# Kernel tuning notes

Hardware: AMD Instinct MI355X
Metric: run time of the kernel (lower is better)

## Reference

```python
import jax, jax.numpy as jnp
import numpy as np

TOP_K = 2
CAPACITY_FACTOR = 1.0


def _ffn(x, w1, w2):
    # SwiGLU FFN: x [N, D], w1 [D, 2F], w2 [F, D]
    h = x @ w1
    x1, x2 = jnp.split(h, 2, axis=-1)
    return (x1 * jax.nn.silu(x2)) @ w2


def setup_inputs() -> dict:
    key = jax.random.key(0)
    ks = jax.random.split(key, 6)
    B, S, D, F, E_r, E_s = 4, 2048, 2048, 1024, 7, 1
    sc_in = 1.0 / np.sqrt(D)
    sc_mid = 1.0 / np.sqrt(F)
    return {
        "x": jax.random.normal(ks[0], (B, S, D), dtype=jnp.float32),
        "gate_w": jax.random.normal(ks[1], (D, E_r), dtype=jnp.float32) * sc_in,
        "expert_bias": jnp.zeros((E_r,), dtype=jnp.float32),
        "shared_w1": jax.random.normal(ks[2], (E_s, D, 2 * F), dtype=jnp.float32) * sc_in,
        "shared_w2": jax.random.normal(ks[3], (E_s, F, D), dtype=jnp.float32) * sc_mid,
        "routed_w1": jax.random.normal(ks[4], (E_r, D, 2 * F), dtype=jnp.float32) * sc_in,
        "routed_w2": jax.random.normal(ks[5], (E_r, F, D), dtype=jnp.float32) * sc_mid,
    }


def reference(x, gate_w, expert_bias, shared_w1, shared_w2, routed_w1, routed_w2):
    B, S, D = x.shape
    E_r = gate_w.shape[1]
    T = B * S
    capacity = max(1, int(CAPACITY_FACTOR * T / E_r))
    flat_x = x.reshape(T, D)

    # shared experts: applied to every token, summed
    shared_sum = jax.vmap(_ffn, in_axes=(None, 0, 0))(flat_x, shared_w1, shared_w2).sum(0)

    # gating (eval mode: no noise, no dropout)
    gate_logits = flat_x @ gate_w + expert_bias  # [T, E_r]
    aff = jax.nn.sigmoid(gate_logits)
    _, topk_idx = jax.lax.top_k(aff, TOP_K)  # [T, K]
    # mask[t, e] = expert e is among token t's top-k
    mask = (topk_idx[:, :, None] == jnp.arange(E_r)[None, None, :]).any(axis=1)  # [T, E_r]

    # per-expert capacity selection: keep top-`capacity` masked tokens by affinity
    score = jnp.where(mask, aff, -1.0).T  # [E_r, T]; aff >= 0 so -1 sorts last
    _, sel_idx = jax.lax.top_k(score, capacity)  # [E_r, capacity] token ids
    kept = jnp.take_along_axis(mask.T, sel_idx, axis=1)  # [E_r, cap]
    w = jnp.where(kept, jnp.take_along_axis(aff.T, sel_idx, axis=1), 0.0)  # [E_r, cap]

    # grouped gather -> FFN -> weighted scatter-add
    inp = flat_x[sel_idx]  # [E_r, cap, D]
    out = jax.vmap(_ffn)(inp, routed_w1, routed_w2)  # [E_r, cap, D]
    routed_sum = jnp.zeros_like(flat_x).at[sel_idx].add(out * w[:, :, None])

    return (shared_sum + routed_sum).reshape(B, S, D)
```

## Files before the change

kernel.cpp:

```cpp
#include <hip/hip_runtime.h>
#include <hip/hip_bf16.h>

typedef unsigned long long u64;
typedef __bf16 bf16x8 __attribute__((ext_vector_type(8)));
typedef float f32x4 __attribute__((ext_vector_type(4)));
typedef unsigned short ushort8_t __attribute__((ext_vector_type(8)));

#define TOKS 8192
#define DMODEL 2048
#define FD 1024
#define NEXP 7
#define CAP 1170
#define CAPP 1280

#define MFMA16(a, b, c) __builtin_amdgcn_mfma_f32_16x16x32_bf16(a, b, c, 0, 0, 0)

__device__ __forceinline__ unsigned short f2bf(float f) {
  __hip_bfloat16 b = __float2bfloat16(f);
  return __builtin_bit_cast(unsigned short, b);
}
__device__ __forceinline__ float bf2f(unsigned short u) {
  __hip_bfloat16 b = __builtin_bit_cast(__hip_bfloat16, u);
  return __bfloat162float(b);
}
__device__ __forceinline__ void gload_lds16(const void* g, void* l) {
  __builtin_amdgcn_global_load_lds(
      (const __attribute__((address_space(1))) void*)g,
      (__attribute__((address_space(3))) void*)l, 16, 0, 0);
}

__global__ void k_convert_x(const float* __restrict__ x,
                            unsigned short* __restrict__ xb, long n4) {
  long i = (long)blockIdx.x * blockDim.x + threadIdx.x;
  long stride = (long)gridDim.x * blockDim.x;
  for (; i < n4; i += stride) {
    float4 v = ((const float4*)x)[i];
    ushort4 o;
    o.x = f2bf(v.x); o.y = f2bf(v.y); o.z = f2bf(v.z); o.w = f2bf(v.w);
    ((ushort4*)xb)[i] = o;
  }
}

template <bool PERM>
__global__ void k_transpose_bf16(const float* __restrict__ in0,
                                 const float* __restrict__ inr,
                                 unsigned short* __restrict__ out,
                                 int R, int C) {
  __shared__ float tile[32][33];
  int z = blockIdx.z;
  const float* in = (z == 0) ? in0 : (inr + (long)(z - 1) * R * C);
  unsigned short* o = out + (long)z * R * C;
  int c0 = blockIdx.x * 32;
  int r0 = blockIdx.y * 32;
  int tx = threadIdx.x, ty = threadIdx.y;
#pragma unroll
  for (int k = 0; k < 4; ++k)
    tile[ty + 8 * k][tx] = in[(long)(r0 + ty + 8 * k) * C + c0 + tx];
  __syncthreads();
#pragma unroll
  for (int k = 0; k < 4; ++k) {
    int c = c0 + ty + 8 * k;
    long orow = PERM ? (long)(((c & 1023) >> 4) * 32 + ((c >> 10) << 4) + (c & 15))
                     : (long)c;
    o[orow * R + r0 + tx] = f2bf(tile[tx][ty + 8 * k]);
  }
}

__global__ void k_gating(const float* __restrict__ x,
                         const float* __restrict__ gw,
                         const float* __restrict__ bias,
                         u64* __restrict__ keys) {
  int wave = threadIdx.x >> 6;
  int lane = threadIdx.x & 63;
  int t = blockIdx.x * 4 + wave;
  const float* xr = x + (long)t * DMODEL;
  double acc[NEXP];
#pragma unroll
  for (int e = 0; e < NEXP; ++e) acc[e] = 0.0;
  for (int i = lane; i < DMODEL; i += 64) {
    double xv = (double)xr[i];
    const float* g = gw + (long)i * NEXP;
#pragma unroll
    for (int e = 0; e < NEXP; ++e) acc[e] += xv * (double)g[e];
  }
#pragma unroll
  for (int e = 0; e < NEXP; ++e) {
    for (int off = 32; off > 0; off >>= 1)
      acc[e] += __shfl_down(acc[e], off, 64);
  }
  if (lane == 0) {
    float aff[NEXP];
#pragma unroll
    for (int e = 0; e < NEXP; ++e) {
      double lg = acc[e] + (double)bias[e];
      aff[e] = (float)(1.0 / (1.0 + exp(-lg)));
    }
    int i1 = 0;
    for (int e = 1; e < NEXP; ++e) if (aff[e] > aff[i1]) i1 = e;
    int i2 = -1;
    for (int e = 0; e < NEXP; ++e) {
      if (e == i1) continue;
      if (i2 < 0 || aff[e] > aff[i2]) i2 = e;
    }
#pragma unroll
    for (int e = 0; e < NEXP; ++e) {
      u64 key = (u64)(0xFFFFFFFFu - (unsigned)t);
      if (e == i1 || e == i2) key |= ((u64)__float_as_uint(aff[e])) << 32;
      keys[(long)e * TOKS + t] = key;
    }
  }
}

__global__ __launch_bounds__(1024) void k_select(
    const u64* __restrict__ keys, int* __restrict__ sel,
    float* __restrict__ selw) {
  __shared__ unsigned hist[256];
  __shared__ u64 s_prefix;
  __shared__ unsigned s_k;
  __shared__ unsigned s_cnt;
  const int e = blockIdx.x;
  const u64* kk = keys + (long)e * TOKS;
  const int tid = threadIdx.x;
  if (tid == 0) { s_prefix = 0; s_k = CAP; s_cnt = 0; }
  __syncthreads();
  for (int shift = 56; shift >= 0; shift -= 8) {
    if (tid < 256) hist[tid] = 0;
    __syncthreads();
    u64 pref = s_prefix;
    for (int i = tid; i < TOKS; i += 1024) {
      u64 key = kk[i];
      bool match = (shift == 56) || ((key >> (shift + 8)) == pref);
      if (match) atomicAdd(&hist[(unsigned)(key >> shift) & 255u], 1u);
    }
    __syncthreads();
    if (tid == 0) {
      unsigned k = s_k, cum = 0;
      for (int b = 255; b >= 0; --b) {
        unsigned c = hist[b];
        if (cum + c >= k) {
          s_prefix = (s_prefix << 8) | (unsigned)b;
          s_k = k - cum;
          break;
        }
        cum += c;
      }
    }
    __syncthreads();
  }
  const u64 T = s_prefix;
  for (int i = tid; i < TOKS; i += 1024) {
    u64 key = kk[i];
    if (key >= T) {
      unsigned p = atomicAdd(&s_cnt, 1u);
      int tok = (int)(0xFFFFFFFFu - (unsigned)(key & 0xFFFFFFFFull));
      unsigned vb = (unsigned)(key >> 32);
      sel[e * CAPP + p] = tok;
      selw[e * CAPP + p] = vb ? __uint_as_float(vb) : 0.0f;
    }
  }
  for (int i = CAP + tid; i < CAPP; i += 1024) {
    sel[e * CAPP + i] = 0;
    selw[e * CAPP + i] = 0.0f;
  }
}

template <int EPI, bool GATHER>
__global__ __launch_bounds__(512, 2) void k_gemm2ph(
    const unsigned short* __restrict__ Abase,
    const unsigned short* __restrict__ Bbase,
    unsigned short* __restrict__ Cbf, float* __restrict__ Cf32,
    const int* __restrict__ sel, const float* __restrict__ selw,
    int N, int K, long strideA, long strideB, long strideC) {
  extern __shared__ unsigned short lds[];
  const int tid = threadIdx.x;
  const int w = tid >> 6;
  const int lane = tid & 63;

  long lin = blockIdx.x + (long)gridDim.x * (blockIdx.y + (long)gridDim.y * blockIdx.z);
  long nwg = (long)gridDim.x * gridDim.y * gridDim.z;
  long swz = (lin & 7) * (nwg >> 3) + (lin >> 3);
  int bx = (int)(swz % gridDim.x);
  long rem = swz / gridDim.x;
  int by = (int)(rem % gridDim.y);
  int z = (int)(rem / gridDim.y);

  const long m0 = (long)by * 256;
  const long n0 = (long)bx * 256;
  const unsigned short* A = Abase + (GATHER ? 0L : (long)z * strideA);
  const unsigned short* Bm = Bbase + (long)z * strideB;

  const int wr = w >> 2;
  const int wc = w & 3;
  const int lr = lane & 15;
  const int kq = lane >> 4;

  const int srow = (w << 3) + (lane >> 3);
  const int scol = (((lane & 7) ^ (lane >> 3)) << 3);
  const unsigned short* aPtr[4];
  const unsigned short* bPtr[4];
#pragma unroll
  for (int j = 0; j < 4; ++j) {
    int r = j * 64 + srow;
    long ar = GATHER ? (long)sel[z * CAPP + (int)m0 + r] : (m0 + r);
    aPtr[j] = A + ar * (long)K + scol;
    bPtr[j] = Bm + (n0 + r) * (long)K + scol;
  }
  const int dst0 = tid * 8;

  auto STAGE = [&](int buf, int t) {
    unsigned short* base = lds + buf * 32768;
    const long ko = (long)t * 64;
#pragma unroll
    for (int j = 0; j < 4; ++j) {
      gload_lds16(aPtr[j] + ko, base + j * 4096 + dst0);
      gload_lds16(bPtr[j] + ko, base + 16384 + j * 4096 + dst0);
    }
  };

  const int slot0 = (kq ^ (lr & 7)) * 8;
  const int slot1 = ((kq + 4) ^ (lr & 7)) * 8;
  const int aRow = wr * 128 + lr;
  const int bRow = wc * 64 + lr;

  const int nk = K >> 6;

  STAGE(0, 0);
  asm volatile("s_waitcnt vmcnt(0)" ::: "memory");
  __builtin_amdgcn_sched_barrier(0);
  __builtin_amdgcn_s_barrier();
  __builtin_amdgcn_sched_barrier(0);

  f32x4 acc[8][4] = {};
  int cur = 0;

#pragma unroll 1
  for (int t = 0; t < nk; ++t) {
    if (t + 1 < nk) STAGE(cur ^ 1, t + 1);
    const unsigned short* aSeg = lds + cur * 32768;
    const unsigned short* bSeg = aSeg + 16384;
    bf16x8 af[8], bf[4];
#pragma unroll
    for (int m = 0; m < 8; ++m)
      af[m] = *(const bf16x8*)&aSeg[(aRow + m * 16) * 64 + slot0];
#pragma unroll
    for (int n = 0; n < 4; ++n)
      bf[n] = *(const bf16x8*)&bSeg[(bRow + n * 16) * 64 + slot0];
    asm volatile("s_waitcnt lgkmcnt(0)" ::: "memory");
    __builtin_amdgcn_sched_barrier(0);
    __builtin_amdgcn_s_setprio(1);
#pragma unroll
    for (int m = 0; m < 8; ++m)
#pragma unroll
      for (int n = 0; n < 4; ++n)
        acc[m][n] = MFMA16(af[m], bf[n], acc[m][n]);
    __builtin_amdgcn_s_setprio(0);
#pragma unroll
    for (int m = 0; m < 8; ++m)
      af[m] = *(const bf16x8*)&aSeg[(aRow + m * 16) * 64 + slot1];
#pragma unroll
    for (int n = 0; n < 4; ++n)
      bf[n] = *(const bf16x8*)&bSeg[(bRow + n * 16) * 64 + slot1];
    asm volatile("s_waitcnt lgkmcnt(0)" ::: "memory");
    __builtin_amdgcn_sched_barrier(0);
    __builtin_amdgcn_s_setprio(1);
#pragma unroll
    for (int m = 0; m < 8; ++m)
#pragma unroll
      for (int n = 0; n < 4; ++n)
        acc[m][n] = MFMA16(af[m], bf[n], acc[m][n]);
    __builtin_amdgcn_s_setprio(0);
    asm volatile("s_waitcnt vmcnt(0)" ::: "memory");
    __builtin_amdgcn_sched_barrier(0);
    __builtin_amdgcn_s_barrier();
    __builtin_amdgcn_sched_barrier(0);
    cur ^= 1;
  }

  const int r0q = (lane >> 4) * 4;
  const int cc = lane & 15;
  const long crow0 = m0 + wr * 128;
  const long ccol0 = n0 + wc * 64;

  if (EPI == 1) {
#pragma unroll
    for (int m = 0; m < 8; ++m)
#pragma unroll
      for (int r = 0; r < 4; ++r) {
        long row = crow0 + m * 16 + r0q + r;
#pragma unroll
        for (int n = 0; n < 4; ++n)
          Cf32[row * N + ccol0 + n * 16 + cc] = acc[m][n][r];
      }
  } else if (EPI == 2) {
#pragma unroll
    for (int m = 0; m < 8; ++m)
#pragma unroll
      for (int r = 0; r < 4; ++r) {
        int srowi = (int)crow0 + m * 16 + r0q + r;
        int tok = sel[z * CAPP + srowi];
        float wgt = selw[z * CAPP + srowi];
        if (wgt != 0.0f) {
#pragma unroll
          for (int n = 0; n < 4; ++n)
            atomicAdd(&Cf32[(long)tok * N + ccol0 + n * 16 + cc],
                      acc[m][n][r] * wgt);
        }
      }
  } else {
    unsigned short* C = Cbf + (long)z * strideC;
    const int halfN = N >> 1;
    const long gcol0 = (ccol0 >> 1);
#pragma unroll
    for (int m = 0; m < 8; ++m)
#pragma unroll
      for (int r = 0; r < 4; ++r) {
        long row = crow0 + m * 16 + r0q + r;
#pragma unroll
        for (int q = 0; q < 2; ++q) {
          float x1v = acc[m][2 * q][r];
          float x2v = acc[m][2 * q + 1][r];
          float s = x2v / (1.0f + __expf(-x2v));
          C[row * halfN + gcol0 + q * 16 + cc] = f2bf(x1v * s);
        }
      }
  }
}

extern "C" void kernel_launch(void* const* d_in, const int* in_sizes, int n_in,
                              void* d_out, int out_size, void* d_ws,
                              size_t ws_size, hipStream_t stream) {
  (void)in_sizes; (void)n_in; (void)out_size; (void)ws_size;
  const float* x = (const float*)d_in[0];
  const float* gw = (const float*)d_in[1];
  const float* eb = (const float*)d_in[2];
  const float* sw1 = (const float*)d_in[3];
  const float* sw2 = (const float*)d_in[4];
  const float* rw1 = (const float*)d_in[5];
  const float* rw2 = (const float*)d_in[6];
  float* out = (float*)d_out;

  char* ws = (char*)d_ws;
  size_t off = 0;
  auto alloc = [&](size_t bytes) {
    size_t o = off;
    off += (bytes + 255) & ~(size_t)255;
    return o;
  };
  unsigned short* xb  = (unsigned short*)(ws + alloc((size_t)TOKS * DMODEL * 2));
  unsigned short* w1t = (unsigned short*)(ws + alloc((size_t)8 * DMODEL * (2 * FD) * 2));
  unsigned short* w2t = (unsigned short*)(ws + alloc((size_t)8 * DMODEL * FD * 2));
  unsigned short* a_sh = (unsigned short*)(ws + alloc((size_t)TOKS * FD * 2));
  unsigned short* a_r  = (unsigned short*)(ws + alloc((size_t)NEXP * CAPP * FD * 2));
  u64* keys = (u64*)(ws + alloc((size_t)NEXP * TOKS * 8));
  int* sel  = (int*)(ws + alloc((size_t)NEXP * CAPP * 4));
  float* selw = (float*)(ws + alloc((size_t)NEXP * CAPP * 4));

  const size_t LDSB = 131072;

  k_convert_x<<<8192, 256, 0, stream>>>(x, xb, (long)TOKS * DMODEL / 4);
  dim3 tb(32, 8);
  k_transpose_bf16<true><<<dim3(64, 64, 8), tb, 0, stream>>>(sw1, rw1, w1t, DMODEL, 2 * FD);
  k_transpose_bf16<false><<<dim3(64, 32, 8), tb, 0, stream>>>(sw2, rw2, w2t, FD, DMODEL);
  k_gating<<<TOKS / 4, 256, 0, stream>>>(x, gw, eb, keys);
  k_select<<<NEXP, 1024, 0, stream>>>(keys, sel, selw);
  k_gemm2ph<3, false><<<dim3(8, 32, 1), 512, LDSB, stream>>>(
      xb, w1t, a_sh, nullptr, nullptr, nullptr, 2 * FD, DMODEL, 0, 0, 0);
  k_gemm2ph<1, false><<<dim3(8, 32, 1), 512, LDSB, stream>>>(
      a_sh, w2t, nullptr, out, nullptr, nullptr, DMODEL, FD, 0, 0, 0);
  k_gemm2ph<3, true><<<dim3(8, CAPP / 256, NEXP), 512, LDSB, stream>>>(
      xb, w1t + (size_t)DMODEL * (2 * FD), a_r, nullptr, sel, nullptr, 2 * FD,
      DMODEL, 0, (long)DMODEL * (2 * FD), (long)CAPP * FD);
  k_gemm2ph<2, false><<<dim3(8, CAPP / 256, NEXP), 512, LDSB, stream>>>(
      a_r, w2t + (size_t)DMODEL * FD, nullptr, out, sel, selw, DMODEL, FD,
      (long)CAPP * FD, (long)DMODEL * FD, 0);
}
```

Measured before the change: 531.2 us.

## Shrink GEMM tiles to 128x128 and replace atomic scatter with deterministic combine

The GEMM kernel moves from 256x256 tiles with 512 threads and 128KB of dynamic LDS to 128x128 tiles with 256 threads, a K-step of 32 and static LDS, so more blocks fit per CU and the grids get more blocks. The routed down-projection no longer atomically adds weighted rows into the output. It writes weighted bf16 rows to a buffer. k_select now builds a per-token inverse map, and a new combine kernel adds the one or two routed rows into the output. This trades scattered fp32 atomics for an extra write and read pass plus a memset, and it rounds the routed outputs to bf16 before they are summed.

```diff
diff --git a/kernel.cpp b/kernel.cpp
--- a/kernel.cpp
+++ b/kernel.cpp
@@ -113,7 +113,8 @@
 
 __global__ __launch_bounds__(1024) void k_select(
     const u64* __restrict__ keys, int* __restrict__ sel,
-    float* __restrict__ selw) {
+    float* __restrict__ selw, unsigned* __restrict__ cnt,
+    int* __restrict__ inv) {
   __shared__ unsigned hist[256];
   __shared__ u64 s_prefix;
   __shared__ unsigned s_k;
@@ -156,6 +157,10 @@
       unsigned vb = (unsigned)(key >> 32);
       sel[e * CAPP + p] = tok;
       selw[e * CAPP + p] = vb ? __uint_as_float(vb) : 0.0f;
+      if (vb) {
+        unsigned pos = atomicAdd(&cnt[tok], 1u);
+        inv[tok * 2 + pos] = e * CAPP + (int)p;
+      }
     }
   }
   for (int i = CAP + tid; i < CAPP; i += 1024) {
@@ -164,14 +169,41 @@
   }
 }
 
+__global__ __launch_bounds__(256) void k_combine(
+    float* __restrict__ out, const unsigned short* __restrict__ rout,
+    const int* __restrict__ inv, const unsigned* __restrict__ cnt) {
+  const int tok = blockIdx.x;
+  const unsigned c = cnt[tok];
+  if (c == 0) return;
+  int i0 = inv[tok * 2];
+  int i1 = (c > 1) ? inv[tok * 2 + 1] : -1;
+  if (c > 1 && i1 < i0) { int t = i0; i0 = i1; i1 = t; }
+  const int col = threadIdx.x * 8;
+  float* o = out + (long)tok * DMODEL + col;
+  float4 v0 = *(float4*)o;
+  float4 v1 = *(float4*)(o + 4);
+  ushort8_t r0 = *(const ushort8_t*)&rout[(long)i0 * DMODEL + col];
+#pragma unroll
+  for (int j = 0; j < 4; ++j) { v0.x; }
+  v0.x += bf2f(r0[0]); v0.y += bf2f(r0[1]); v0.z += bf2f(r0[2]); v0.w += bf2f(r0[3]);
+  v1.x += bf2f(r0[4]); v1.y += bf2f(r0[5]); v1.z += bf2f(r0[6]); v1.w += bf2f(r0[7]);
+  if (c > 1) {
+    ushort8_t r1 = *(const ushort8_t*)&rout[(long)i1 * DMODEL + col];
+    v0.x += bf2f(r1[0]); v0.y += bf2f(r1[1]); v0.z += bf2f(r1[2]); v0.w += bf2f(r1[3]);
+    v1.x += bf2f(r1[4]); v1.y += bf2f(r1[5]); v1.z += bf2f(r1[6]); v1.w += bf2f(r1[7]);
+  }
+  *(float4*)o = v0;
+  *(float4*)(o + 4) = v1;
+}
+
 template <int EPI, bool GATHER>
-__global__ __launch_bounds__(512, 2) void k_gemm2ph(
+__global__ __launch_bounds__(256, 4) void k_gemm128(
     const unsigned short* __restrict__ Abase,
     const unsigned short* __restrict__ Bbase,
     unsigned short* __restrict__ Cbf, float* __restrict__ Cf32,
     const int* __restrict__ sel, const float* __restrict__ selw,
     int N, int K, long strideA, long strideB, long strideC) {
-  extern __shared__ unsigned short lds[];
+  __shared__ unsigned short lds[2][8192];
   const int tid = threadIdx.x;
   const int w = tid >> 6;
   const int lane = tid & 63;
@@ -184,45 +216,45 @@
   int by = (int)(rem % gridDim.y);
   int z = (int)(rem / gridDim.y);
 
-  const long m0 = (long)by * 256;
-  const long n0 = (long)bx * 256;
+  const long m0 = (long)by * 128;
+  const long n0 = (long)bx * 128;
   const unsigned short* A = Abase + (GATHER ? 0L : (long)z * strideA);
   const unsigned short* Bm = Bbase + (long)z * strideB;
 
-  const int wr = w >> 2;
-  const int wc = w & 3;
+  const int wr = w >> 1;
+  const int wc = w & 1;
   const int lr = lane & 15;
   const int kq = lane >> 4;
 
-  const int srow = (w << 3) + (lane >> 3);
-  const int scol = (((lane & 7) ^ (lane >> 3)) << 3);
-  const unsigned short* aPtr[4];
-  const unsigned short* bPtr[4];
-#pragma unroll
-  for (int j = 0; j < 4; ++j) {
-    int r = j * 64 + srow;
+  const int r_ = (w << 4) + (lane >> 2);
+  const int p_ = lane & 3;
+  const unsigned short* aSrc[2];
+  const unsigned short* bSrc[2];
+#pragma unroll
+  for (int c = 0; c < 2; ++c) {
+    int r = c * 64 + r_;
+    int q = p_ ^ ((r & 3) ^ ((r >> 2) & 3));
     long ar = GATHER ? (long)sel[z * CAPP + (int)m0 + r] : (m0 + r);
-    aPtr[j] = A + ar * (long)K + scol;
-    bPtr[j] = Bm + (n0 + r) * (long)K + scol;
+    aSrc[c] = A + ar * (long)K + q * 8;
+    bSrc[c] = Bm + (n0 + r) * (long)K + q * 8;
   }
   const int dst0 = tid * 8;
 
   auto STAGE = [&](int buf, int t) {
-    unsigned short* base = lds + buf * 32768;
-    const long ko = (long)t * 64;
-#pragma unroll
-    for (int j = 0; j < 4; ++j) {
-      gload_lds16(aPtr[j] + ko, base + j * 4096 + dst0);
-      gload_lds16(bPtr[j] + ko, base + 16384 + j * 4096 + dst0);
+    const long ko = (long)t * 32;
+#pragma unroll
+    for (int c = 0; c < 2; ++c) {
+      gload_lds16(aSrc[c] + ko, &lds[buf][c * 2048 + dst0]);
+      gload_lds16(bSrc[c] + ko, &lds[buf][4096 + c * 2048 + dst0]);
     }
   };
 
-  const int slot0 = (kq ^ (lr & 7)) * 8;
-  const int slot1 = ((kq + 4) ^ (lr & 7)) * 8;
-  const int aRow = wr * 128 + lr;
+  const int gl = (lr & 3) ^ ((lr >> 2) & 3);
+  const int slot = (kq ^ gl) * 8;
+  const int aRow = wr * 64 + lr;
   const int bRow = wc * 64 + lr;
 
-  const int nk = K >> 6;
+  const int nk = K >> 5;
 
   STAGE(0, 0);
   asm volatile("s_waitcnt vmcnt(0)" ::: "memory");
@@ -230,41 +262,26 @@
   __builtin_amdgcn_s_barrier();
   __builtin_amdgcn_sched_barrier(0);
 
-  f32x4 acc[8][4] = {};
+  f32x4 acc[4][4] = {};
   int cur = 0;
 
 #pragma unroll 1
   for (int t = 0; t < nk; ++t) {
     if (t + 1 < nk) STAGE(cur ^ 1, t + 1);
-    const unsigned short* aSeg = lds + cur * 32768;
-    const unsigned short* bSeg = aSeg + 16384;
-    bf16x8 af[8], bf[4];
-#pragma unroll
-    for (int m = 0; m < 8; ++m)
-      af[m] = *(const bf16x8*)&aSeg[(aRow + m * 16) * 64 + slot0];
+    const unsigned short* aSeg = &lds[cur][0];
+    const unsigned short* bSeg = &lds[cur][4096];
+    bf16x8 af[4], bf[4];
+#pragma unroll
+    for (int m = 0; m < 4; ++m)
+      af[m] = *(const bf16x8*)&aSeg[(aRow + m * 16) * 32 + slot];
 #pragma unroll
     for (int n = 0; n < 4; ++n)
-      bf[n] = *(const bf16x8*)&bSeg[(bRow + n * 16) * 64 + slot0];
+      bf[n] = *(const bf16x8*)&bSeg[(bRow + n * 16) * 32 + slot];
     asm volatile("s_waitcnt lgkmcnt(0)" ::: "memory");
     __builtin_amdgcn_sched_barrier(0);
     __builtin_amdgcn_s_setprio(1);
 #pragma unroll
-    for (int m = 0; m < 8; ++m)
-#pragma unroll
-      for (int n = 0; n < 4; ++n)
-        acc[m][n] = MFMA16(af[m], bf[n], acc[m][n]);
-    __builtin_amdgcn_s_setprio(0);
-#pragma unroll
-    for (int m = 0; m < 8; ++m)
-      af[m] = *(const bf16x8*)&aSeg[(aRow + m * 16) * 64 + slot1];
-#pragma unroll
-    for (int n = 0; n < 4; ++n)
-      bf[n] = *(const bf16x8*)&bSeg[(bRow + n * 16) * 64 + slot1];
-    asm volatile("s_waitcnt lgkmcnt(0)" ::: "memory");
-    __builtin_amdgcn_sched_barrier(0);
-    __builtin_amdgcn_s_setprio(1);
-#pragma unroll
-    for (int m = 0; m < 8; ++m)
+    for (int m = 0; m < 4; ++m)
 #pragma unroll
       for (int n = 0; n < 4; ++n)
         acc[m][n] = MFMA16(af[m], bf[n], acc[m][n]);
@@ -278,12 +295,12 @@
 
   const int r0q = (lane >> 4) * 4;
   const int cc = lane & 15;
-  const long crow0 = m0 + wr * 128;
+  const long crow0 = m0 + wr * 64;
   const long ccol0 = n0 + wc * 64;
 
   if (EPI == 1) {
 #pragma unroll
-    for (int m = 0; m < 8; ++m)
+    for (int m = 0; m < 4; ++m)
 #pragma unroll
       for (int r = 0; r < 4; ++r) {
         long row = crow0 + m * 16 + r0q + r;
@@ -291,27 +308,12 @@
         for (int n = 0; n < 4; ++n)
           Cf32[row * N + ccol0 + n * 16 + cc] = acc[m][n][r];
       }
-  } else if (EPI == 2) {
-#pragma unroll
-    for (int m = 0; m < 8; ++m)
-#pragma unroll
-      for (int r = 0; r < 4; ++r) {
-        int srowi = (int)crow0 + m * 16 + r0q + r;
-        int tok = sel[z * CAPP + srowi];
-        float wgt = selw[z * CAPP + srowi];
-        if (wgt != 0.0f) {
-#pragma unroll
-          for (int n = 0; n < 4; ++n)
-            atomicAdd(&Cf32[(long)tok * N + ccol0 + n * 16 + cc],
-                      acc[m][n][r] * wgt);
-        }
-      }
-  } else {
+  } else if (EPI == 3) {
     unsigned short* C = Cbf + (long)z * strideC;
     const int halfN = N >> 1;
     const long gcol0 = (ccol0 >> 1);
 #pragma unroll
-    for (int m = 0; m < 8; ++m)
+    for (int m = 0; m < 4; ++m)
 #pragma unroll
       for (int r = 0; r < 4; ++r) {
         long row = crow0 + m * 16 + r0q + r;
@@ -322,6 +324,18 @@
           float s = x2v / (1.0f + __expf(-x2v));
           C[row * halfN + gcol0 + q * 16 + cc] = f2bf(x1v * s);
         }
+      }
+  } else {
+#pragma unroll
+    for (int m = 0; m < 4; ++m)
+#pragma unroll
+      for (int r = 0; r < 4; ++r) {
+        int rloc = (int)crow0 + m * 16 + r0q + r;
+        float wgt = selw[z * CAPP + rloc];
+        unsigned short* C = Cbf + ((long)z * CAPP + rloc) * N;
+#pragma unroll
+        for (int n = 0; n < 4; ++n)
+          C[ccol0 + n * 16 + cc] = f2bf(acc[m][n][r] * wgt);
       }
   }
 }
@@ -351,26 +365,29 @@
   unsigned short* w2t = (unsigned short*)(ws + alloc((size_t)8 * DMODEL * FD * 2));
   unsigned short* a_sh = (unsigned short*)(ws + alloc((size_t)TOKS * FD * 2));
   unsigned short* a_r  = (unsigned short*)(ws + alloc((size_t)NEXP * CAPP * FD * 2));
+  unsigned short* r_out = (unsigned short*)(ws + alloc((size_t)NEXP * CAPP * DMODEL * 2));
   u64* keys = (u64*)(ws + alloc((size_t)NEXP * TOKS * 8));
   int* sel  = (int*)(ws + alloc((size_t)NEXP * CAPP * 4));
   float* selw = (float*)(ws + alloc((size_t)NEXP * CAPP * 4));
-
-  const size_t LDSB = 131072;
+  unsigned* cnt = (unsigned*)(ws + alloc((size_t)TOKS * 4));
+  int* inv = (int*)(ws + alloc((size_t)TOKS * 2 * 4));
 
   k_convert_x<<<8192, 256, 0, stream>>>(x, xb, (long)TOKS * DMODEL / 4);
   dim3 tb(32, 8);
   k_transpose_bf16<true><<<dim3(64, 64, 8), tb, 0, stream>>>(sw1, rw1, w1t, DMODEL, 2 * FD);
   k_transpose_bf16<false><<<dim3(64, 32, 8), tb, 0, stream>>>(sw2, rw2, w2t, FD, DMODEL);
   k_gating<<<TOKS / 4, 256, 0, stream>>>(x, gw, eb, keys);
-  k_select<<<NEXP, 1024, 0, stream>>>(keys, sel, selw);
-  k_gemm2ph<3, false><<<dim3(8, 32, 1), 512, LDSB, stream>>>(
+  hipMemsetAsync(cnt, 0, (size_t)TOKS * 4, stream);
+  k_select<<<NEXP, 1024, 0, stream>>>(keys, sel, selw, cnt, inv);
+  k_gemm128<3, false><<<dim3(16, 64, 1), 256, 0, stream>>>(
       xb, w1t, a_sh, nullptr, nullptr, nullptr, 2 * FD, DMODEL, 0, 0, 0);
-  k_gemm2ph<1, false><<<dim3(8, 32, 1), 512, LDSB, stream>>>(
+  k_gemm128<1, false><<<dim3(16, 64, 1), 256, 0, stream>>>(
       a_sh, w2t, nullptr, out, nullptr, nullptr, DMODEL, FD, 0, 0, 0);
-  k_gemm2ph<3, true><<<dim3(8, CAPP / 256, NEXP), 512, LDSB, stream>>>(
+  k_gemm128<3, true><<<dim3(16, CAPP / 128, NEXP), 256, 0, stream>>>(
       xb, w1t + (size_t)DMODEL * (2 * FD), a_r, nullptr, sel, nullptr, 2 * FD,
       DMODEL, 0, (long)DMODEL * (2 * FD), (long)CAPP * FD);
-  k_gemm2ph<2, false><<<dim3(8, CAPP / 256, NEXP), 512, LDSB, stream>>>(
-      a_r, w2t + (size_t)DMODEL * FD, nullptr, out, sel, selw, DMODEL, FD,
+  k_gemm128<4, false><<<dim3(16, CAPP / 128, NEXP), 256, 0, stream>>>(
+      a_r, w2t + (size_t)DMODEL * FD, r_out, nullptr, sel, selw, DMODEL, FD,
       (long)CAPP * FD, (long)DMODEL * FD, 0);
-}
+  k_combine<<<TOKS, 256, 0, stream>>>(out, r_out, inv, cnt);
+}
```

Measured after the change: 518.3 us. 1.02x faster.
